# Kernel tuning notes

Measured on AMD Instinct MI355X. Metric: run time of the kernel, lower is better.

Reference implementation:

```python
import jax, jax.numpy as jnp
import numpy as np

N = 500      # nodes
F = 32       # input features
H = 128      # hidden_dim
HEADS = 2
B = 4        # batch
T = 16       # time steps
E = 8000     # edges (before self loops)
BN_EPS = 1e-5


def setup_inputs() -> dict:
    key = jax.random.key(0)
    ks = jax.random.split(key, 16)
    r = lambda i, shp, s=0.1: jax.random.normal(ks[i], shp, jnp.float32) * s
    return {
        "x": jax.random.normal(ks[0], (B, T, N, F), jnp.float32),
        "edge_index": jax.random.randint(ks[1], (2, E), 0, N),
        "W_proj": r(2, (F, H)), "b_proj": jnp.zeros((H,), jnp.float32),
        "gat1_Wl": r(3, (F, HEADS * H)), "gat1_Wr": r(4, (F, HEADS * H)),
        "gat1_att": r(5, (HEADS, H)), "gat1_b": jnp.zeros((HEADS * H,), jnp.float32),
        "bn1_g": jnp.ones((HEADS * H,), jnp.float32), "bn1_b": jnp.zeros((HEADS * H,), jnp.float32),
        "gat2_Wl": r(6, (HEADS * H, H)), "gat2_Wr": r(7, (HEADS * H, H)),
        "gat2_att": r(8, (1, H)), "gat2_b": jnp.zeros((H,), jnp.float32),
        "bn2_g": jnp.ones((H,), jnp.float32), "bn2_b": jnp.zeros((H,), jnp.float32),
        "Wih0": r(9, (4 * H, H)), "Whh0": r(10, (4 * H, H)),
        "bih0": jnp.zeros((4 * H,), jnp.float32), "bhh0": jnp.zeros((4 * H,), jnp.float32),
        "Wih1": r(11, (4 * H, H)), "Whh1": r(12, (4 * H, H)),
        "bih1": jnp.zeros((4 * H,), jnp.float32), "bhh1": jnp.zeros((4 * H,), jnp.float32),
        "fc_W1": r(13, (H, H // 2)), "fc_b1": jnp.zeros((H // 2,), jnp.float32),
        "fc_W2": r(14, (H // 2, 1)), "fc_b2": jnp.zeros((1,), jnp.float32),
    }


def gatv2(h, src, dst, Wl, Wr, att, bias, heads, out_dim, concat):
    # h: [G, N, Fin]; edges src -> dst (PyG convention), self loops included.
    G, n, _ = h.shape
    xl = (h @ Wl).reshape(G, n, heads, out_dim)
    xr = (h @ Wr).reshape(G, n, heads, out_dim)
    e = jax.nn.leaky_relu(xl[:, src] + xr[:, dst], 0.2)        # [G,E,heads,C]
    logits = jnp.einsum('gehc,hc->geh', e, att)                # [G,E,heads]
    m = jnp.full((G, n, heads), -jnp.inf, logits.dtype).at[:, dst].max(logits)
    ex = jnp.exp(logits - m[:, dst])
    s = jnp.zeros((G, n, heads), logits.dtype).at[:, dst].add(ex)
    alpha = ex / (s[:, dst] + 1e-16)
    msg = xl[:, src] * alpha[..., None]                        # [G,E,heads,C]
    out = jnp.zeros((G, n, heads, out_dim), h.dtype).at[:, dst].add(msg)
    out = out.reshape(G, n, heads * out_dim) if concat else out.mean(axis=2)
    return out + bias


def batchnorm(h, g, b):
    # BatchNorm1d in training mode: stats over the node axis, per graph call.
    mean = h.mean(axis=1, keepdims=True)
    var = jnp.var(h, axis=1, keepdims=True)
    return (h - mean) * jax.lax.rsqrt(var + BN_EPS) * g + b


def lstm_layer(xs, Wih, Whh, bih, bhh):
    # xs: [T, BN, H] -> ys: [T, BN, H]; torch gate order i,f,g,o.
    BNsz = xs.shape[1]
    h0 = jnp.zeros((BNsz, H), xs.dtype)
    def step(carry, xt):
        h, c = carry
        gates = xt @ Wih.T + h @ Whh.T + bih + bhh
        i, f, g, o = jnp.split(gates, 4, axis=-1)
        c = jax.nn.sigmoid(f) * c + jax.nn.sigmoid(i) * jnp.tanh(g)
        h = jax.nn.sigmoid(o) * jnp.tanh(c)
        return (h, c), h
    _, ys = jax.lax.scan(step, (h0, h0), xs)
    return ys


def reference(x, edge_index, W_proj, b_proj, gat1_Wl, gat1_Wr, gat1_att, gat1_b,
              bn1_g, bn1_b, gat2_Wl, gat2_Wr, gat2_att, gat2_b, bn2_g, bn2_b,
              Wih0, Whh0, bih0, bhh0, Wih1, Whh1, bih1, bhh1,
              fc_W1, fc_b1, fc_W2, fc_b2):
    b, t, n, f = x.shape
    G = b * t
    loops = jnp.arange(n, dtype=edge_index.dtype)  # GATv2Conv add_self_loops=True
    src = jnp.concatenate([edge_index[0], loops])
    dst = jnp.concatenate([edge_index[1], loops])
    xg = x.reshape(G, n, f)  # fuse all (b,t) graph calls into one batched pass
    h = gatv2(xg, src, dst, gat1_Wl, gat1_Wr, gat1_att, gat1_b, HEADS, H, True)
    h = jax.nn.elu(batchnorm(h, bn1_g, bn1_b))  # dropout = identity (eval)
    h = gatv2(h, src, dst, gat2_Wl, gat2_Wr, gat2_att, gat2_b, 1, H, False)
    h = jax.nn.elu(batchnorm(h, bn2_g, bn2_b))
    h = h + (xg @ W_proj + b_proj)               # residual input projection
    # faithful to torch: spatial.view(b*n, t, H) is a raw reshape of [b,t,n,H]
    flat = h.reshape(b * n, t, H)
    xs = jnp.swapaxes(flat, 0, 1)                # [t, b*n, H]
    ys = lstm_layer(xs, Wih0, Whh0, bih0, bhh0)
    ys = lstm_layer(ys, Wih1, Whh1, bih1, bhh1)  # inter-layer dropout = identity
    last = ys[-1]                                # [b*n, H]
    out = jax.nn.relu(last @ fc_W1 + fc_b1) @ fc_W2 + fc_b2
    return out.reshape(b, n, -1)
```

## Files before the change

### kernel.cpp

```cpp
#include <hip/hip_runtime.h>
#include <hip/hip_bf16.h>
#include <math.h>

#define G_   64
#define NN_  500
#define FIN_ 32
#define HD_  128
#define C1_  256
#define E0_  8000
#define EP_  8500
#define TT_  16
#define NR_  2000

typedef __attribute__((ext_vector_type(8))) short bf16x8;
typedef __attribute__((ext_vector_type(4))) float f32x4;

__device__ __forceinline__ float fsig(float x)  { return 1.f / (1.f + __expf(-x)); }
__device__ __forceinline__ float ftanh(float x) {
    float e = __expf(fminf(fmaxf(2.f * x, -30.f), 30.f));
    return (e - 1.f) / (e + 1.f);
}
__device__ __forceinline__ unsigned short f2bf(float f) {
    unsigned int u = __float_as_uint(f);
    return (unsigned short)((u + 0x7FFFu + ((u >> 16) & 1u)) >> 16);
}
__device__ __forceinline__ float bf2f(unsigned short h) {
    return __uint_as_float(((unsigned int)h) << 16);
}

__global__ __launch_bounds__(512) void k_degscan(const int* __restrict__ ei,
                                                 int* __restrict__ rowptr, int* __restrict__ cursor) {
    __shared__ int degs[512];
    __shared__ int scan[512];
    int t = threadIdx.x;
    degs[t] = 0;
    __syncthreads();
    for (int e = t; e < EP_; e += 512) {
        int dst = e < E0_ ? ei[E0_ + e] : e - E0_;
        atomicAdd(&degs[dst], 1);
    }
    __syncthreads();
    int v = degs[t];
    scan[t] = v;
    __syncthreads();
    for (int off = 1; off < 512; off <<= 1) {
        int add = (t >= off) ? scan[t - off] : 0;
        __syncthreads();
        scan[t] += add;
        __syncthreads();
    }
    int ex = scan[t] - v;
    if (t < NN_) { rowptr[t] = ex; cursor[t] = ex; }
    if (t == NN_) rowptr[NN_] = ex;
}
__global__ void k_fill(const int* __restrict__ ei, int* __restrict__ cursor, int* __restrict__ eids) {
    int e = blockIdx.x * blockDim.x + threadIdx.x;
    if (e >= EP_) return;
    int dst = e < E0_ ? ei[E0_ + e] : e - E0_;
    int pos = atomicAdd(&cursor[dst], 1);
    eids[pos] = e;
}

__global__ void k_wt(const float* __restrict__ Whh0, const float* __restrict__ Wih0,
                     const float* __restrict__ Whh1, const float* __restrict__ Wih1,
                     unsigned short* __restrict__ WB0, unsigned short* __restrict__ WB1) {
    int layer = blockIdx.y;
    int n = blockIdx.x * 256 + threadIdx.x;
    const float* Wh = layer ? Whh1 : Whh0;
    const float* Wi = layer ? Wih1 : Wih0;
    unsigned short* WB = layer ? WB1 : WB0;
    int j = n & 7, col = (n >> 3) & 511, kb8 = n >> 12;
    int k = kb8 * 8 + j;
    float w = (k < 128) ? Wh[(size_t)col * 128 + k] : Wi[(size_t)col * 128 + (k - 128)];
    unsigned short h = f2bf(w);
    WB[n] = h;
    WB[131072 + n] = f2bf(w - bf2f(h));
}

__global__ void k_wtg(const float* __restrict__ Wl1, const float* __restrict__ Wr1,
                      const float* __restrict__ Wp,  const float* __restrict__ W2l,
                      const float* __restrict__ W2r, unsigned short* __restrict__ out) {
    int t = blockIdx.x * 256 + threadIdx.x;
    if (t >= 86016) return;
    const float* W; int N, base, local, KN;
    if (t < 8192)       { W = Wl1; N = 256; base = 0;      local = t;         KN = 8192;  }
    else if (t < 16384) { W = Wr1; N = 256; base = 16384;  local = t - 8192;  KN = 8192;  }
    else if (t < 20480) { W = Wp;  N = 128; base = 32768;  local = t - 16384; KN = 4096;  }
    else if (t < 53248) { W = W2l; N = 128; base = 40960;  local = t - 20480; KN = 32768; }
    else                { W = W2r; N = 128; base = 106496; local = t - 53248; KN = 32768; }
    int k = local / N, n = local - k * N;
    float wv = W[local];
    int idx = ((k >> 3) * N + n) * 8 + (k & 7);
    unsigned short h = f2bf(wv);
    out[base + idx] = h;
    out[base + KN + idx] = f2bf(wv - bf2f(h));
}

__global__ __launch_bounds__(256) void k_mm1(
    const float* __restrict__ x, const unsigned short* __restrict__ WP,
    const float* __restrict__ bp,
    float* __restrict__ xl1, float* __restrict__ xr1, float* __restrict__ proj)
{
    int tid = threadIdx.x, lane = tid & 63, w = tid >> 6;
    int row = lane & 15, kg = lane >> 4;
    int rb = blockIdx.x * 64 + w * 16;
    const float* ap = &x[(size_t)(rb + row) * 32 + kg * 8];
    float4 a0 = *(const float4*)ap, a1 = *(const float4*)(ap + 4);
    union { unsigned short u[8]; bf16x8 v; } ah, al;
    {
        float av[8] = {a0.x,a0.y,a0.z,a0.w,a1.x,a1.y,a1.z,a1.w};
        #pragma unroll
        for (int j = 0; j < 8; ++j) {
            unsigned short hb = f2bf(av[j]);
            ah.u[j] = hb;
            al.u[j] = f2bf(av[j] - bf2f(hb));
        }
    }
    const int crow = kg * 4;
    #pragma unroll 4
    for (int nt = 0; nt < 16; ++nt) {
        int n = nt * 16 + row;
        int idx = (kg * 256 + n) * 8;
        bf16x8 bh = *(const bf16x8*)(WP + idx);
        bf16x8 bl = *(const bf16x8*)(WP + 8192 + idx);
        f32x4 acc = {0.f,0.f,0.f,0.f};
        acc = __builtin_amdgcn_mfma_f32_16x16x32_bf16(ah.v, bh, acc, 0, 0, 0);
        acc = __builtin_amdgcn_mfma_f32_16x16x32_bf16(al.v, bh, acc, 0, 0, 0);
        acc = __builtin_amdgcn_mfma_f32_16x16x32_bf16(ah.v, bl, acc, 0, 0, 0);
        #pragma unroll
        for (int r = 0; r < 4; ++r)
            xl1[(size_t)(rb + crow + r) * 256 + n] = acc[r];
    }
    #pragma unroll 4
    for (int nt = 0; nt < 16; ++nt) {
        int n = nt * 16 + row;
        int idx = (kg * 256 + n) * 8;
        bf16x8 bh = *(const bf16x8*)(WP + 16384 + idx);
        bf16x8 bl = *(const bf16x8*)(WP + 24576 + idx);
        f32x4 acc = {0.f,0.f,0.f,0.f};
        acc = __builtin_amdgcn_mfma_f32_16x16x32_bf16(ah.v, bh, acc, 0, 0, 0);
        acc = __builtin_amdgcn_mfma_f32_16x16x32_bf16(al.v, bh, acc, 0, 0, 0);
        acc = __builtin_amdgcn_mfma_f32_16x16x32_bf16(ah.v, bl, acc, 0, 0, 0);
        #pragma unroll
        for (int r = 0; r < 4; ++r)
            xr1[(size_t)(rb + crow + r) * 256 + n] = acc[r];
    }
    #pragma unroll 4
    for (int nt = 0; nt < 8; ++nt) {
        int n = nt * 16 + row;
        int idx = (kg * 128 + n) * 8;
        bf16x8 bh = *(const bf16x8*)(WP + 32768 + idx);
        bf16x8 bl = *(const bf16x8*)(WP + 36864 + idx);
        f32x4 acc = {0.f,0.f,0.f,0.f};
        acc = __builtin_amdgcn_mfma_f32_16x16x32_bf16(ah.v, bh, acc, 0, 0, 0);
        acc = __builtin_amdgcn_mfma_f32_16x16x32_bf16(al.v, bh, acc, 0, 0, 0);
        acc = __builtin_amdgcn_mfma_f32_16x16x32_bf16(ah.v, bl, acc, 0, 0, 0);
        float bv = bp[n];
        #pragma unroll
        for (int r = 0; r < 4; ++r)
            proj[(size_t)(rb + crow + r) * 128 + n] = acc[r] + bv;
    }
}

__global__ __launch_bounds__(512) void k_mm2(
    const float* __restrict__ h1, const unsigned short* __restrict__ WP,
    const float* __restrict__ sc1, const float* __restrict__ sh1,
    float* __restrict__ xl2, float* __restrict__ xr2)
{
    int tid = threadIdx.x, lane = tid & 63, w = tid >> 6;
    int wr = w >> 2, wc = w & 3;
    int row = lane & 15, kg = lane >> 4;
    int rb = blockIdx.x * 32 + wr * 16;
    int grow = rb + row;
    int g = grow / NN_;
    const float* scp = sc1 + g * 256;
    const float* shp = sh1 + g * 256;
    const int cb = wc * 32 + row;
    f32x4 aL0 = {0.f,0.f,0.f,0.f}, aL1 = {0.f,0.f,0.f,0.f};
    f32x4 aR0 = {0.f,0.f,0.f,0.f}, aR1 = {0.f,0.f,0.f,0.f};
    #pragma unroll 2
    for (int kt = 0; kt < 8; ++kt) {
        int k0 = kt * 32 + kg * 8;
        const float* hp = &h1[(size_t)grow * 256 + k0];
        float4 h0 = *(const float4*)hp, h4 = *(const float4*)(hp + 4);
        float4 s0 = *(const float4*)&scp[k0], s4 = *(const float4*)&scp[k0 + 4];
        float4 t0 = *(const float4*)&shp[k0], t4 = *(const float4*)&shp[k0 + 4];
        union { unsigned short u[8]; bf16x8 v; } ah, al;
        {
            float hv[8] = {h0.x,h0.y,h0.z,h0.w,h4.x,h4.y,h4.z,h4.w};
            float sv[8] = {s0.x,s0.y,s0.z,s0.w,s4.x,s4.y,s4.z,s4.w};
            float tv[8] = {t0.x,t0.y,t0.z,t0.w,t4.x,t4.y,t4.z,t4.w};
            #pragma unroll
            for (int j = 0; j < 8; ++j) {
                float v = hv[j] * sv[j] + tv[j];
                v = v > 0.f ? v : expm1f(v);
                unsigned short hb = f2bf(v);
                ah.u[j] = hb;
                al.u[j] = f2bf(v - bf2f(hb));
            }
        }
        int idx = ((kt * 4 + kg) * 128 + cb) * 8;
        bf16x8 bhL0 = *(const bf16x8*)(WP + 40960 + idx);
        bf16x8 blL0 = *(const bf16x8*)(WP + 73728 + idx);
        bf16x8 bhL1 = *(const bf16x8*)(WP + 40960 + idx + 128);
        bf16x8 blL1 = *(const bf16x8*)(WP + 73728 + idx + 128);
        bf16x8 bhR0 = *(const bf16x8*)(WP + 106496 + idx);
        bf16x8 blR0 = *(const bf16x8*)(WP + 139264 + idx);
        bf16x8 bhR1 = *(const bf16x8*)(WP + 106496 + idx + 128);
        bf16x8 blR1 = *(const bf16x8*)(WP + 139264 + idx + 128);
        aL0 = __builtin_amdgcn_mfma_f32_16x16x32_bf16(ah.v, bhL0, aL0, 0, 0, 0);
        aL0 = __builtin_amdgcn_mfma_f32_16x16x32_bf16(al.v, bhL0, aL0, 0, 0, 0);
        aL0 = __builtin_amdgcn_mfma_f32_16x16x32_bf16(ah.v, blL0, aL0, 0, 0, 0);
        aL1 = __builtin_amdgcn_mfma_f32_16x16x32_bf16(ah.v, bhL1, aL1, 0, 0, 0);
        aL1 = __builtin_amdgcn_mfma_f32_16x16x32_bf16(al.v, bhL1, aL1, 0, 0, 0);
        aL1 = __builtin_amdgcn_mfma_f32_16x16x32_bf16(ah.v, blL1, aL1, 0, 0, 0);
        aR0 = __builtin_amdgcn_mfma_f32_16x16x32_bf16(ah.v, bhR0, aR0, 0, 0, 0);
        aR0 = __builtin_amdgcn_mfma_f32_16x16x32_bf16(al.v, bhR0, aR0, 0, 0, 0);
        aR0 = __builtin_amdgcn_mfma_f32_16x16x32_bf16(ah.v, blR0, aR0, 0, 0, 0);
        aR1 = __builtin_amdgcn_mfma_f32_16x16x32_bf16(ah.v, bhR1, aR1, 0, 0, 0);
        aR1 = __builtin_amdgcn_mfma_f32_16x16x32_bf16(al.v, bhR1, aR1, 0, 0, 0);
        aR1 = __builtin_amdgcn_mfma_f32_16x16x32_bf16(ah.v, blR1, aR1, 0, 0, 0);
    }
    const int crow = kg * 4;
    #pragma unroll
    for (int r = 0; r < 4; ++r) {
        size_t orow = (size_t)(rb + crow + r);
        xl2[orow * 128 + wc * 32 + row]      = aL0[r];
        xl2[orow * 128 + wc * 32 + 16 + row] = aL1[r];
        xr2[orow * 128 + wc * 32 + row]      = aR0[r];
        xr2[orow * 128 + wc * 32 + 16 + row] = aR1[r];
    }
}

template<int NH, int CD>
__global__ __launch_bounds__(256) void k_gat(
    const float* __restrict__ xl, const float* __restrict__ xr,
    const float* __restrict__ att, const int* __restrict__ ei,
    const int* __restrict__ rowptr, const int* __restrict__ eids,
    const float* __restrict__ bias, float* __restrict__ out)
{
    const int BD = NH * CD;
    const int NC = BD / 64;
    int bs = (blockIdx.x & 7) * 1000 + (blockIdx.x >> 3);
    int wid = bs * 4 + (threadIdx.x >> 6);
    int lane = threadIdx.x & 63;
    if (wid >= G_ * NN_) return;
    int g = wid / NN_, dst = wid % NN_;
    size_t gbase = (size_t)g * NN_;
    int ch0 = lane * NC;

    float xr_[NC], att_[NC], acc[NC];
    {
        const float* xrp = &xr[(gbase + dst) * BD + ch0];
        #pragma unroll
        for (int j = 0; j < NC; ++j) { xr_[j] = xrp[j]; att_[j] = att[ch0 + j]; acc[j] = 0.f; }
    }
    float m = -1e30f, ssum = 0.f;
    int rs = rowptr[dst], re = rowptr[dst + 1];
    int efull = rs + ((re - rs) & ~3);

#define LOADROW(IDX, DSTV) { \
        int eid_ = eids[IDX]; \
        int src_ = eid_ < E0_ ? ei[eid_] : eid_ - E0_; \
        const float* xp_ = &xl[(gbase + src_) * BD + ch0]; \
        if constexpr (NC == 4) { float4 t_ = *(const float4*)xp_; DSTV[0]=t_.x; DSTV[1]=t_.y; DSTV[2]=t_.z; DSTV[3]=t_.w; } \
        else { float2 t_ = *(const float2*)xp_; DSTV[0]=t_.x; DSTV[1]=t_.y; } \
    }

    int i = rs;
    if (i < efull) {
        float n0[NC], n1[NC], n2[NC], n3[NC];
        LOADROW(i + 0, n0); LOADROW(i + 1, n1); LOADROW(i + 2, n2); LOADROW(i + 3, n3);
        while (i < efull) {
            float r0[NC], r1[NC], r2[NC], r3[NC];
            #pragma unroll
            for (int j = 0; j < NC; ++j) { r0[j]=n0[j]; r1[j]=n1[j]; r2[j]=n2[j]; r3[j]=n3[j]; }
            i += 4;
            if (i < efull) {
                LOADROW(i + 0, n0); LOADROW(i + 1, n1); LOADROW(i + 2, n2); LOADROW(i + 3, n3);
            }
            float p0 = 0.f, p1 = 0.f, p2 = 0.f, p3 = 0.f;
            #pragma unroll
            for (int j = 0; j < NC; ++j) {
                float v0 = r0[j] + xr_[j]; v0 = v0 > 0.f ? v0 : 0.2f * v0; p0 = fmaf(v0, att_[j], p0);
                float v1 = r1[j] + xr_[j]; v1 = v1 > 0.f ? v1 : 0.2f * v1; p1 = fmaf(v1, att_[j], p1);
                float v2 = r2[j] + xr_[j]; v2 = v2 > 0.f ? v2 : 0.2f * v2; p2 = fmaf(v2, att_[j], p2);
                float v3 = r3[j] + xr_[j]; v3 = v3 > 0.f ? v3 : 0.2f * v3; p3 = fmaf(v3, att_[j], p3);
            }
            #pragma unroll
            for (int o = (NH == 2 ? 16 : 32); o; o >>= 1) {
                p0 += __shfl_xor(p0, o);
                p1 += __shfl_xor(p1, o);
                p2 += __shfl_xor(p2, o);
                p3 += __shfl_xor(p3, o);
            }
            float gm = fmaxf(fmaxf(p0, p1), fmaxf(p2, p3));
            float nm = fmaxf(m, gm);
            float fo = __expf(m - nm);
            float e0 = __expf(p0 - nm), e1 = __expf(p1 - nm);
            float e2 = __expf(p2 - nm), e3 = __expf(p3 - nm);
            #pragma unroll
            for (int j = 0; j < NC; ++j)
                acc[j] = acc[j] * fo + e0 * r0[j] + e1 * r1[j] + e2 * r2[j] + e3 * r3[j];
            ssum = ssum * fo + (e0 + e1 + e2 + e3);
            m = nm;
        }
    }
    for (; i < re; ++i) {
        float cu[NC];
        LOADROW(i, cu);
        float p = 0.f;
        #pragma unroll
        for (int j = 0; j < NC; ++j) {
            float v = cu[j] + xr_[j];
            v = v > 0.f ? v : 0.2f * v;
            p = fmaf(v, att_[j], p);
        }
        #pragma unroll
        for (int o = (NH == 2 ? 16 : 32); o; o >>= 1) p += __shfl_xor(p, o);
        float nm = fmaxf(m, p);
        float fo = __expf(m - nm), en = __expf(p - nm);
        #pragma unroll
        for (int j = 0; j < NC; ++j) acc[j] = acc[j] * fo + en * cu[j];
        ssum = ssum * fo + en;
        m = nm;
    }
#undef LOADROW
    float inv = 1.f / (ssum + 1e-16f);
    float* op = &out[(gbase + dst) * BD + ch0];
    #pragma unroll
    for (int j = 0; j < NC; ++j) op[j] = acc[j] * inv + bias[ch0 + j];
}

template<int C>
__global__ __launch_bounds__(C * 4) void k_bnstats(
    const float* __restrict__ h, const float* __restrict__ gamma, const float* __restrict__ beta,
    float* __restrict__ scale, float* __restrict__ shift)
{
    int g = blockIdx.x;
    int c = threadIdx.x % C, q = threadIdx.x / C;
    __shared__ float ps[4][C], pss[4][C];
    float s = 0.f, ss = 0.f;
    for (int n = q * 125; n < (q + 1) * 125; ++n) {
        float v = h[((size_t)g * NN_ + n) * C + c];
        s += v; ss += v * v;
    }
    ps[q][c] = s; pss[q][c] = ss;
    __syncthreads();
    if (q == 0) {
        #pragma unroll
        for (int qq = 1; qq < 4; ++qq) { s += ps[qq][c]; ss += pss[qq][c]; }
        float m = s * (1.f / NN_);
        float var = ss * (1.f / NN_) - m * m;
        float r = rsqrtf(var + 1e-5f);
        float sc = r * gamma[c];
        scale[g * C + c] = sc;
        shift[g * C + c] = beta[c] - m * sc;
    }
}

__global__ void k_bn_elu_add4(const float* __restrict__ h2, const float* __restrict__ scale2,
                              const float* __restrict__ shift2, const float* __restrict__ proj,
                              float* __restrict__ hres) {
    int i4 = blockIdx.x * blockDim.x + threadIdx.x;
    if (i4 >= G_ * NN_ * HD_ / 4) return;
    int base = i4 * 4;
    int c = base & 127;
    int g = base / (NN_ * HD_);
    float4 hv = *(const float4*)&h2[base];
    float4 sc = *(const float4*)&scale2[g * 128 + c];
    float4 sh = *(const float4*)&shift2[g * 128 + c];
    float4 pv = *(const float4*)&proj[base];
    float v0 = hv.x * sc.x + sh.x; v0 = (v0 > 0.f ? v0 : expm1f(v0)) + pv.x;
    float v1 = hv.y * sc.y + sh.y; v1 = (v1 > 0.f ? v1 : expm1f(v1)) + pv.y;
    float v2 = hv.z * sc.z + sh.z; v2 = (v2 > 0.f ? v2 : expm1f(v2)) + pv.z;
    float v3 = hv.w * sc.w + sh.w; v3 = (v3 > 0.f ? v3 : expm1f(v3)) + pv.w;
    *(float4*)&hres[base] = make_float4(v0, v1, v2, v3);
}

#define GROW 516

__device__ __forceinline__ void mfma_gates16(
    const bf16x8* __restrict__ Fh_hi, const bf16x8* __restrict__ Fh_lo,
    const bf16x8* __restrict__ Fx_hi, const bf16x8* __restrict__ Fx_lo,
    const unsigned short* __restrict__ WB, float* __restrict__ gl,
    const float* __restrict__ bb, int lane, int w)
{
    f32x4 acc[2] = {{0.f,0.f,0.f,0.f},{0.f,0.f,0.f,0.f}};
    const int row = lane & 15, kg = lane >> 4;
    const int cb = w * 32 + row;
    #pragma unroll 2
    for (int kt = 0; kt < 8; ++kt) {
        const bf16x8* Hh = (kt < 4) ? Fh_hi : Fx_hi;
        const bf16x8* Hl = (kt < 4) ? Fh_lo : Fx_lo;
        int fu = ((kt & 3) * 4 + kg) * 16 + row;
        bf16x8 ah = Hh[fu];
        bf16x8 al = Hl[fu];
        const unsigned short* ph = WB + ((size_t)(kt * 4 + kg) * 512 + cb) * 8;
        #pragma unroll
        for (int nt = 0; nt < 2; ++nt) {
            bf16x8 bh = *(const bf16x8*)(ph + nt * 128);
            bf16x8 bl = *(const bf16x8*)(ph + 131072 + nt * 128);
            acc[nt] = __builtin_amdgcn_mfma_f32_16x16x32_bf16(ah, bh, acc[nt], 0, 0, 0);
            acc[nt] = __builtin_amdgcn_mfma_f32_16x16x32_bf16(al, bh, acc[nt], 0, 0, 0);
            acc[nt] = __builtin_amdgcn_mfma_f32_16x16x32_bf16(ah, bl, acc[nt], 0, 0, 0);
        }
    }
    const int crow = kg * 4;
    #pragma unroll
    for (int nt = 0; nt < 2; ++nt)
        #pragma unroll
        for (int r = 0; r < 4; ++r)
            gl[(crow + r) * GROW + w * 32 + nt * 16 + row] = acc[nt][r] + bb[nt];
}

__device__ __forceinline__ void cell_frag(
    const float* __restrict__ gl, float* __restrict__ cs,
    bf16x8* __restrict__ Hhi, bf16x8* __restrict__ Hlo, int t256)
{
    int r = t256 & 15, kb8 = t256 >> 4;
    const float* gr = gl + r * GROW + kb8 * 8;
    float* cp = cs + (r * 128 + kb8 * 8);
    union { unsigned short u[8]; bf16x8 v; } hh, hl;
    float cv[8];
    #pragma unroll
    for (int j = 0; j < 8; ++j) {
        float iv = fsig(gr[j]);
        float fv = fsig(gr[128 + j]);
        float gv = ftanh(gr[256 + j]);
        float ov = fsig(gr[384 + j]);
        float cn = fv * cp[j] + iv * gv;
        cv[j] = cn;
        float hv = ov * ftanh(cn);
        unsigned short hb = f2bf(hv);
        hh.u[j] = hb;
        hl.u[j] = f2bf(hv - bf2f(hb));
    }
    #pragma unroll
    for (int j = 0; j < 8; ++j) cp[j] = cv[j];
    Hhi[t256] = hh.v;
    Hlo[t256] = hl.v;
}

__device__ __forceinline__ void stage_x_frag(
    const float* __restrict__ src_row,
    bf16x8* __restrict__ Xhi, bf16x8* __restrict__ Xlo, int t256)
{
    int kb8 = t256 >> 4;
    const float* sp = src_row + kb8 * 8;
    union { unsigned short u[8]; bf16x8 v; } hh, hl;
    #pragma unroll
    for (int j = 0; j < 8; ++j) {
        float v = sp[j];
        unsigned short hb = f2bf(v);
        hh.u[j] = hb;
        hl.u[j] = f2bf(v - bf2f(hb));
    }
    Xhi[t256] = hh.v;
    Xlo[t256] = hl.v;
}

__global__ __launch_bounds__(1024, 4) void k_lstm_all(
    const float* __restrict__ hres,
    const unsigned short* __restrict__ WB0, const unsigned short* __restrict__ WB1,
    const float* __restrict__ bih0, const float* __restrict__ bhh0,
    const float* __restrict__ bih1, const float* __restrict__ bhh1,
    const float* __restrict__ fcW1, const float* __restrict__ fcb1,
    const float* __restrict__ fcW2, const float* __restrict__ fcb2,
    float* __restrict__ out)
{
    __shared__ bf16x8 h1h[256], h1l[256], h2h[256], h2l[256], xh[256], xlo[256];
    __shared__ float c1s[16 * 128], c2s[16 * 128];
    __shared__ float gl[16 * GROW];
    int tid = threadIdx.x, lane = tid & 63, w = tid >> 6;
    int r0 = blockIdx.x * 16;

    if (tid < 256) {
        bf16x8 z = {0,0,0,0,0,0,0,0};
        h1h[tid] = z; h1l[tid] = z; h2h[tid] = z; h2l[tid] = z;
    }
    for (int i = tid; i < 16 * 128; i += 1024) { c1s[i] = 0.f; c2s[i] = 0.f; }

    float bb0[2], bb1[2];
    #pragma unroll
    for (int nt = 0; nt < 2; ++nt) {
        int c = w * 32 + nt * 16 + (lane & 15);
        bb0[nt] = bih0[c] + bhh0[c];
        bb1[nt] = bih1[c] + bhh1[c];
    }
    if (tid >= 768) {
        int t256 = tid - 768;
        int r = t256 & 15;
        stage_x_frag(&hres[(size_t)((r0 + r) * 16 + 0) * 128], xh, xlo, t256);
    }
    __syncthreads();
    for (int t = 0; t < TT_; ++t) {
        mfma_gates16(h1h, h1l, xh, xlo, WB0, gl, bb0, lane, w);
        __syncthreads();
        if (tid < 256) cell_frag(gl, c1s, h1h, h1l, tid);
        __syncthreads();
        mfma_gates16(h2h, h2l, h1h, h1l, WB1, gl, bb1, lane, w);
        __syncthreads();
        if (tid < 256) {
            cell_frag(gl, c2s, h2h, h2l, tid);
        } else if (tid >= 768 && t < TT_ - 1) {
            int t256 = tid - 768;
            int r = t256 & 15;
            stage_x_frag(&hres[(size_t)((r0 + r) * 16 + t + 1) * 128], xh, xlo, t256);
        }
        __syncthreads();
    }
    if (tid < 512) {
        const unsigned short* h2hu = (const unsigned short*)h2h;
        const unsigned short* h2lu = (const unsigned short*)h2l;
        int fr = tid >> 5, j = tid & 31;
        float s0 = fcb1[j], s1 = fcb1[j + 32];
        #pragma unroll 8
        for (int k = 0; k < 128; ++k) {
            int fi = ((k >> 3) * 16 + fr) * 8 + (k & 7);
            float hv = bf2f(h2hu[fi]) + bf2f(h2lu[fi]);
            s0 += hv * fcW1[k * 64 + j];
            s1 += hv * fcW1[k * 64 + j + 32];
        }
        float p = fmaxf(s0, 0.f) * fcW2[j] + fmaxf(s1, 0.f) * fcW2[j + 32];
        #pragma unroll
        for (int o = 16; o; o >>= 1) p += __shfl_xor(p, o);
        if (j == 0) out[r0 + fr] = p + fcb2[0];
    }
}

static const size_t OFF_XL1  = 0;
static const size_t OFF_XR1  = 8192000;
static const size_t OFF_H1   = 16384000;
static const size_t OFF_XL2  = 24576000;
static const size_t OFF_XR2  = 28672000;
static const size_t OFF_H2   = 32768000;
static const size_t OFF_PRJ  = 36864000;
static const size_t OFF_HRES = 40960000;
static const size_t OFF_SC1  = 45056000;
static const size_t OFF_SH1  = 45072384;
static const size_t OFF_SC2  = 45088768;
static const size_t OFF_SH2  = 45096960;
static const size_t OFF_WT0  = 45105152;
static const size_t OFF_WT1  = 45236224;
static const size_t OFF_WGP  = 45367296;
static const size_t OFF_INT  = 45453312;

extern "C" void kernel_launch(void* const* d_in, const int* in_sizes, int n_in,
                              void* d_out, int out_size, void* d_ws, size_t ws_size,
                              hipStream_t stream) {
    const float* x        = (const float*)d_in[0];
    const int*   ei       = (const int*)  d_in[1];
    const float* W_proj   = (const float*)d_in[2];
    const float* b_proj   = (const float*)d_in[3];
    const float* gat1_Wl  = (const float*)d_in[4];
    const float* gat1_Wr  = (const float*)d_in[5];
    const float* gat1_att = (const float*)d_in[6];
    const float* gat1_b   = (const float*)d_in[7];
    const float* bn1_g    = (const float*)d_in[8];
    const float* bn1_b    = (const float*)d_in[9];
    const float* gat2_Wl  = (const float*)d_in[10];
    const float* gat2_Wr  = (const float*)d_in[11];
    const float* gat2_att = (const float*)d_in[12];
    const float* gat2_b   = (const float*)d_in[13];
    const float* bn2_g    = (const float*)d_in[14];
    const float* bn2_b    = (const float*)d_in[15];
    const float* Wih0     = (const float*)d_in[16];
    const float* Whh0     = (const float*)d_in[17];
    const float* bih0     = (const float*)d_in[18];
    const float* bhh0     = (const float*)d_in[19];
    const float* Wih1     = (const float*)d_in[20];
    const float* Whh1     = (const float*)d_in[21];
    const float* bih1     = (const float*)d_in[22];
    const float* bhh1     = (const float*)d_in[23];
    const float* fc_W1    = (const float*)d_in[24];
    const float* fc_b1    = (const float*)d_in[25];
    const float* fc_W2    = (const float*)d_in[26];
    const float* fc_b2    = (const float*)d_in[27];
    float* out = (float*)d_out;

    float* ws = (float*)d_ws;
    float* xl1  = ws + OFF_XL1;
    float* xr1  = ws + OFF_XR1;
    float* h1   = ws + OFF_H1;
    float* xl2  = ws + OFF_XL2;
    float* xr2  = ws + OFF_XR2;
    float* h2   = ws + OFF_H2;
    float* proj = ws + OFF_PRJ;
    float* hres = ws + OFF_HRES;
    float* sc1  = ws + OFF_SC1;
    float* sh1  = ws + OFF_SH1;
    float* sc2  = ws + OFF_SC2;
    float* sh2  = ws + OFF_SH2;
    unsigned short* WB0 = (unsigned short*)(ws + OFF_WT0);
    unsigned short* WB1 = (unsigned short*)(ws + OFF_WT1);
    unsigned short* WGP = (unsigned short*)(ws + OFF_WGP);

    int* ibase  = (int*)(ws + OFF_INT);
    int* rowptr = ibase;
    int* cursor = ibase + 512;
    int* eids   = ibase + 1024;

    k_degscan<<<1, 512, 0, stream>>>(ei, rowptr, cursor);
    k_fill<<<(EP_ + 255) / 256, 256, 0, stream>>>(ei, cursor, eids);
    k_wt<<<dim3(512, 2), 256, 0, stream>>>(Whh0, Wih0, Whh1, Wih1, WB0, WB1);
    k_wtg<<<336, 256, 0, stream>>>(gat1_Wl, gat1_Wr, W_proj, gat2_Wl, gat2_Wr, WGP);

    k_mm1<<<500, 256, 0, stream>>>(x, WGP, b_proj, xl1, xr1, proj);
    k_gat<2, HD_><<<8000, 256, 0, stream>>>(xl1, xr1, gat1_att, ei, rowptr, eids, gat1_b, h1);
    k_bnstats<C1_><<<G_, C1_ * 4, 0, stream>>>(h1, bn1_g, bn1_b, sc1, sh1);

    k_mm2<<<1000, 512, 0, stream>>>(h1, WGP, sc1, sh1, xl2, xr2);
    k_gat<1, HD_><<<8000, 256, 0, stream>>>(xl2, xr2, gat2_att, ei, rowptr, eids, gat2_b, h2);
    k_bnstats<HD_><<<G_, HD_ * 4, 0, stream>>>(h2, bn2_g, bn2_b, sc2, sh2);

    k_bn_elu_add4<<<(G_ * NN_ * HD_ / 4 + 255) / 256, 256, 0, stream>>>(h2, sc2, sh2, proj, hres);

    k_lstm_all<<<125, 1024, 0, stream>>>(hres, WB0, WB1, bih0, bhh0, bih1, bhh1,
                                         fc_W1, fc_b1, fc_W2, fc_b2, out);
}
```

Baseline: 419.2 us.

## Wavefront-pipeline the two LSTM layers across warp groups within each step

The fused LSTM kernel now splits its 16 warps into two groups. One group computes layer-0 gates for step t while the other computes layer-1 gates for step t-1, each writing to its own gate buffer. Each warp covers 64 gate columns instead of 32, and the cell updates for both layers plus the x staging run concurrently in one phase. This cuts the barriers per step from four to two and overlaps the two layers' work, at the cost of an extra shared-memory gate buffer, more accumulator registers per warp, and one extra pipeline step.

```diff
diff --git a/kernel.cpp b/kernel.cpp
--- a/kernel.cpp
+++ b/kernel.cpp
@@ -380,15 +380,15 @@
 
 #define GROW 516
 
-__device__ __forceinline__ void mfma_gates16(
+__device__ __forceinline__ void mfma_gates8(
     const bf16x8* __restrict__ Fh_hi, const bf16x8* __restrict__ Fh_lo,
     const bf16x8* __restrict__ Fx_hi, const bf16x8* __restrict__ Fx_lo,
     const unsigned short* __restrict__ WB, float* __restrict__ gl,
-    const float* __restrict__ bb, int lane, int w)
-{
-    f32x4 acc[2] = {{0.f,0.f,0.f,0.f},{0.f,0.f,0.f,0.f}};
+    const float* __restrict__ bb, int lane, int w8)
+{
+    f32x4 acc[4] = {{0.f,0.f,0.f,0.f},{0.f,0.f,0.f,0.f},{0.f,0.f,0.f,0.f},{0.f,0.f,0.f,0.f}};
     const int row = lane & 15, kg = lane >> 4;
-    const int cb = w * 32 + row;
+    const int cb = w8 * 64 + row;
     #pragma unroll 2
     for (int kt = 0; kt < 8; ++kt) {
         const bf16x8* Hh = (kt < 4) ? Fh_hi : Fx_hi;
@@ -398,7 +398,7 @@
         bf16x8 al = Hl[fu];
         const unsigned short* ph = WB + ((size_t)(kt * 4 + kg) * 512 + cb) * 8;
         #pragma unroll
-        for (int nt = 0; nt < 2; ++nt) {
+        for (int nt = 0; nt < 4; ++nt) {
             bf16x8 bh = *(const bf16x8*)(ph + nt * 128);
             bf16x8 bl = *(const bf16x8*)(ph + 131072 + nt * 128);
             acc[nt] = __builtin_amdgcn_mfma_f32_16x16x32_bf16(ah, bh, acc[nt], 0, 0, 0);
@@ -408,10 +408,10 @@
     }
     const int crow = kg * 4;
     #pragma unroll
-    for (int nt = 0; nt < 2; ++nt)
+    for (int nt = 0; nt < 4; ++nt)
         #pragma unroll
         for (int r = 0; r < 4; ++r)
-            gl[(crow + r) * GROW + w * 32 + nt * 16 + row] = acc[nt][r] + bb[nt];
+            gl[(crow + r) * GROW + w8 * 64 + nt * 16 + row] = acc[nt][r] + bb[nt];
 }
 
 __device__ __forceinline__ void cell_frag(
@@ -471,8 +471,9 @@
 {
     __shared__ bf16x8 h1h[256], h1l[256], h2h[256], h2l[256], xh[256], xlo[256];
     __shared__ float c1s[16 * 128], c2s[16 * 128];
-    __shared__ float gl[16 * GROW];
+    __shared__ float glA[16 * GROW], glB[16 * GROW];
     int tid = threadIdx.x, lane = tid & 63, w = tid >> 6;
+    int grp = w >> 3, w8 = w & 7;
     int r0 = blockIdx.x * 16;
 
     if (tid < 256) {
@@ -481,32 +482,35 @@
     }
     for (int i = tid; i < 16 * 128; i += 1024) { c1s[i] = 0.f; c2s[i] = 0.f; }
 
-    float bb0[2], bb1[2];
+    float bbL[4];
     #pragma unroll
-    for (int nt = 0; nt < 2; ++nt) {
-        int c = w * 32 + nt * 16 + (lane & 15);
-        bb0[nt] = bih0[c] + bhh0[c];
-        bb1[nt] = bih1[c] + bhh1[c];
-    }
-    if (tid >= 768) {
-        int t256 = tid - 768;
+    for (int nt = 0; nt < 4; ++nt) {
+        int c = w8 * 64 + nt * 16 + (lane & 15);
+        bbL[nt] = grp ? (bih1[c] + bhh1[c]) : (bih0[c] + bhh0[c]);
+    }
+    if (tid >= 512 && tid < 768) {
+        int t256 = tid - 512;
         int r = t256 & 15;
         stage_x_frag(&hres[(size_t)((r0 + r) * 16 + 0) * 128], xh, xlo, t256);
     }
     __syncthreads();
-    for (int t = 0; t < TT_; ++t) {
-        mfma_gates16(h1h, h1l, xh, xlo, WB0, gl, bb0, lane, w);
-        __syncthreads();
-        if (tid < 256) cell_frag(gl, c1s, h1h, h1l, tid);
-        __syncthreads();
-        mfma_gates16(h2h, h2l, h1h, h1l, WB1, gl, bb1, lane, w);
+    for (int t = 0; t <= TT_; ++t) {
+        if (grp == 0) {
+            if (t < TT_) mfma_gates8(h1h, h1l, xh, xlo, WB0, glA, bbL, lane, w8);
+        } else {
+            if (t >= 1)  mfma_gates8(h2h, h2l, h1h, h1l, WB1, glB, bbL, lane, w8);
+        }
         __syncthreads();
         if (tid < 256) {
-            cell_frag(gl, c2s, h2h, h2l, tid);
-        } else if (tid >= 768 && t < TT_ - 1) {
-            int t256 = tid - 768;
-            int r = t256 & 15;
-            stage_x_frag(&hres[(size_t)((r0 + r) * 16 + t + 1) * 128], xh, xlo, t256);
+            if (t < TT_) cell_frag(glA, c1s, h1h, h1l, tid);
+        } else if (tid < 512) {
+            if (t >= 1)  cell_frag(glB, c2s, h2h, h2l, tid - 256);
+        } else if (tid < 768) {
+            if (t + 1 < TT_) {
+                int t256 = tid - 512;
+                int r = t256 & 15;
+                stage_x_frag(&hres[(size_t)((r0 + r) * 16 + t + 1) * 128], xh, xlo, t256);
+            }
         }
         __syncthreads();
     }
```

After: 413.2 us. About the same (-1.4%).
